# Performance work log

Measured on AMD Instinct MI355X. Metric: run time of the kernel, lower is better.

The kernel has to match this reference:

```python
import jax, jax.numpy as jnp
import numpy as np

V = 50000      # vocab_size
E = 512        # embed_size
H = 512        # hidden_size
B = 128        # batch
S = 256        # encoder seq len
MAX_OOVS = 12


def setup_inputs() -> dict:
    key = jax.random.key(0)
    ks = jax.random.split(key, 18)
    s = 0.05
    embed_table = jax.random.normal(ks[4], (V, E), jnp.float32) * s
    embed_table = embed_table.at[0].set(0.0)  # padding_idx=0
    return {
        'input_idx':   jax.random.randint(ks[0], (B,), 0, V),
        'encoded':     jax.random.normal(ks[1], (B, S, H), jnp.float32),
        'encoded_idx': jax.random.randint(ks[2], (B, S), 0, V),
        'prev_state':  jax.random.normal(ks[3], (B, H), jnp.float32),
        'weighted':    jnp.zeros((B, 1, H), jnp.float32),
        'embed_table': embed_table,
        'Ws_w':    jax.random.normal(ks[5], (H, H), jnp.float32) * s,
        'Ws_b':    jnp.zeros((H,), jnp.float32),
        'gru_Wih': jax.random.normal(ks[6], (3 * H, E + H), jnp.float32) * s,
        'gru_Whh': jax.random.normal(ks[7], (3 * H, H), jnp.float32) * s,
        'gru_bih': jnp.zeros((3 * H,), jnp.float32),
        'gru_bhh': jnp.zeros((3 * H,), jnp.float32),
        'attn_W':  jax.random.normal(ks[8], (H, 2 * H), jnp.float32) * s,
        'attn_b':  jnp.zeros((H,), jnp.float32),
        'attn_v':  jax.random.normal(ks[9], (H,), jnp.float32) * s,
        'Wo_w':    jax.random.normal(ks[10], (V, 2 * H), jnp.float32) * s,
        'Wo_b':    jnp.zeros((V,), jnp.float32),
        'Wc_w':    jax.random.normal(ks[11], (2 * H, H), jnp.float32) * s,
        'Wc_b':    jnp.zeros((2 * H,), jnp.float32),
    }


def copy_decoder_fwd(input_idx, encoded, encoded_idx, prev_state, weighted,
                     embed_table, Ws_w, Ws_b, gru_Wih, gru_Whh, gru_bih, gru_bhh,
                     attn_W, attn_b, attn_v, Wo_w, Wo_b, Wc_w, Wc_b):
    b, seq, hidden = encoded.shape
    vocab = Wo_w.shape[0]
    dt = encoded.dtype

    # order == 0 branch: project prev_state, zero the weighted context
    prev = prev_state @ Ws_w.T + Ws_b                      # (b, h)
    wtd = jnp.zeros((b, hidden), dt)                       # (b, h)

    # GRU single step (PyTorch gate layout: r, z, n)
    x = jnp.concatenate([embed_table[input_idx], wtd], axis=1)  # (b, e+h)
    gi = x @ gru_Wih.T + gru_bih                           # (b, 3h)
    gh = prev @ gru_Whh.T + gru_bhh                        # (b, 3h)
    i_r, i_z, i_n = jnp.split(gi, 3, axis=1)
    h_r, h_z, h_n = jnp.split(gh, 3, axis=1)
    r = jax.nn.sigmoid(i_r + h_r)
    z = jax.nn.sigmoid(i_z + h_z)
    n = jnp.tanh(i_n + r * h_n)
    state = (1.0 - z) * n + z * prev                       # (b, h), == rnn_output

    # 'concat' attention: softmax_seq(v . tanh(W[h; enc] + b))
    h_exp = jnp.broadcast_to(state[:, None, :], (b, seq, hidden))
    energy = jnp.tanh(jnp.concatenate([h_exp, encoded], axis=-1) @ attn_W.T + attn_b)
    attn_w = jax.nn.softmax(energy @ attn_v, axis=1)       # (b, seq)
    context = jnp.einsum('bs,bsh->bh', attn_w, encoded)    # (b, h)

    # generation scores
    score_g = jnp.concatenate([state, context], axis=1) @ Wo_w.T + Wo_b  # (b, V)

    # copy scores
    sc = jnp.tanh(encoded @ Wc_w.T + Wc_b)                 # (b, seq, 2h)
    score_c = jnp.einsum('bsk,bk->bs', sc, jnp.concatenate([state, context], axis=1))
    score_c = score_c + jnp.where(encoded_idx == 0, -1000.0, 0.0).astype(dt)

    # joint softmax over vocab + seq
    probs = jax.nn.softmax(jnp.concatenate([score_g, score_c], axis=1), axis=1)
    prob_g = probs[:, :vocab]                              # (b, V)
    prob_c = probs[:, vocab:]                              # (b, seq)
    prob_c_given = prob_c / jnp.sum(prob_c)                # global-scalar normalization (faithful)

    # pad generation probs with small oov mass
    vext = vocab + MAX_OOVS
    prob_g_ext = jnp.concatenate(
        [prob_g, jnp.full((b, MAX_OOVS), 1e-4, dt)], axis=1)  # (b, V+oov)

    # copy -> vocab scatter-add (replaces dense one-hot + bmm)
    batch_ids = jnp.broadcast_to(jnp.arange(b)[:, None], (b, seq))
    prob_c_to_g = jnp.zeros((b, vext), dt).at[batch_ids, encoded_idx].add(prob_c)

    out = (prob_g_ext + prob_c_to_g)[:, None, :]           # (b, 1, V+oov)

    # positions in source equal to the current input token
    ind = (encoded_idx == input_idx[:, None]).astype(dt)   # (b, seq)
    ssum = ind.sum(axis=1, keepdims=True)
    ind = jnp.where(ssum > 1.0, ind / ssum, ind)
    attn2 = prob_c_given * ind                             # (b, seq)
    weighted_new = jnp.einsum('bs,bsh->bh', attn2, encoded)[:, None, :]  # (b, 1, h)

    return out, state, weighted_new


def reference(input_idx, encoded, encoded_idx, prev_state, weighted,
              embed_table, Ws_w, Ws_b, gru_Wih, gru_Whh, gru_bih, gru_bhh,
              attn_W, attn_b, attn_v, Wo_w, Wo_b, Wc_w, Wc_b):
    return copy_decoder_fwd(input_idx, encoded, encoded_idx, prev_state, weighted,
                            embed_table, Ws_w, Ws_b, gru_Wih, gru_Whh, gru_bih, gru_bhh,
                            attn_W, attn_b, attn_v, Wo_w, Wo_b, Wc_w, Wc_b)
```

## Files before the change

kernel.cpp:

```cpp
#include <hip/hip_runtime.h>
#include <hip/hip_bf16.h>
#include <math.h>

#define BB 128
#define SS 256
#define HH 512
#define VV 50000
#define VEXT 50012

typedef __bf16 bf16x8 __attribute__((ext_vector_type(8)));
typedef float f32x4 __attribute__((ext_vector_type(4)));

__device__ __forceinline__ float fast_tanh(float x) {
  float e = __expf(2.0f * x);
  return 1.0f - 2.0f / (e + 1.0f);
}
__device__ __forceinline__ float fast_sigmoid(float x) {
  return 1.0f / (1.0f + __expf(-x));
}
__device__ __forceinline__ bf16x8 cvt8(const float* p) {
  float4 a = *(const float4*)p;
  float4 b = *(const float4*)(p + 4);
  bf16x8 r;
  r[0] = (__bf16)a.x; r[1] = (__bf16)a.y; r[2] = (__bf16)a.z; r[3] = (__bf16)a.w;
  r[4] = (__bf16)b.x; r[5] = (__bf16)b.y; r[6] = (__bf16)b.z; r[7] = (__bf16)b.w;
  return r;
}

__global__ void k_pack_w(const float* __restrict__ src, int ldw, int coff, int icount,
                         __hip_bfloat16* __restrict__ dst) {
  int i = blockIdx.x * 256 + threadIdx.x;
  if (i >= icount) return;
  int l = i & 63, ks = (i >> 6) & 15, tile = i >> 10;
  int m = l & 15, q = l >> 4;
  const float* p = src + (size_t)(tile * 16 + m) * ldw + coff + ks * 32 + q * 8;
  *(bf16x8*)(dst + (size_t)i * 8) = cvt8(p);
}

__global__ void k_pack_enc(const float* __restrict__ enc, __hip_bfloat16* __restrict__ epk) {
  int i = blockIdx.x * 256 + threadIdx.x;
  int l = i & 63, ks = (i >> 6) & 15, st = (i >> 10) & 15, b = i >> 14;
  int m = l & 15, q = l >> 4;
  const float* p = enc + ((size_t)b * SS + st * 16 + m) * HH + ks * 32 + q * 8;
  *(bf16x8*)(epk + (size_t)i * 8) = cvt8(p);
}

template <int LDB, bool GATHER>
__global__ __launch_bounds__(256, 2) void k_gemm_bt(
    const float* __restrict__ A, const float* __restrict__ B,
    const float* __restrict__ bias, float* __restrict__ C, int ldc,
    const int* __restrict__ gidx) {
  __shared__ __hip_bfloat16 ylds[128 * 72];
  const int t = threadIdx.x;
  const int l = t & 63, w = t >> 6;
  const int m = l & 15, q = l >> 4;
  const int n = blockIdx.x * 64 + w * 16 + m;
  const float* wrow = B + (size_t)n * LDB;
  f32x4 acc[8];
#pragma unroll
  for (int mt = 0; mt < 8; ++mt) acc[mt] = (f32x4){0.f, 0.f, 0.f, 0.f};

  for (int kt = 0; kt < 512; kt += 64) {
    __syncthreads();
#pragma unroll
    for (int i = 0; i < 8; ++i) {
      int f = t + i * 256;
      int row = f >> 4, c4 = f & 15;
      const float* arow;
      if (GATHER)
        arow = A + (size_t)gidx[row] * 512;
      else
        arow = A + (size_t)row * 512;
      float4 v = *(const float4*)(arow + kt + c4 * 4);
      __hip_bfloat16* d = ylds + row * 72 + c4 * 4;
      d[0] = __float2bfloat16(v.x); d[1] = __float2bfloat16(v.y);
      d[2] = __float2bfloat16(v.z); d[3] = __float2bfloat16(v.w);
    }
    __syncthreads();
#pragma unroll
    for (int ksl = 0; ksl < 2; ++ksl) {
      bf16x8 bfr = cvt8(wrow + kt + ksl * 32 + q * 8);
#pragma unroll
      for (int mt = 0; mt < 8; ++mt) {
        bf16x8 af = *(const bf16x8*)(ylds + (mt * 16 + m) * 72 + ksl * 32 + q * 8);
        acc[mt] = __builtin_amdgcn_mfma_f32_16x16x32_bf16(af, bfr, acc[mt], 0, 0, 0);
      }
    }
  }
  float bv = bias[n];
#pragma unroll
  for (int mt = 0; mt < 8; ++mt) {
#pragma unroll
    for (int r = 0; r < 4; ++r) {
      int rowm = mt * 16 + q * 4 + r;
      C[(size_t)rowm * ldc + n] = acc[mt][r] + bv;
    }
  }
}

__global__ void k_gates(const float* __restrict__ gi, const float* __restrict__ gh,
                        const float* __restrict__ prevv, float* __restrict__ state,
                        float* __restrict__ state_out) {
  int i = blockIdx.x * 256 + threadIdx.x;
  int b = i >> 9, h = i & 511;
  const float* gib = gi + (size_t)b * 1536;
  const float* ghb = gh + (size_t)b * 1536;
  float ir = gib[h], iz = gib[512 + h], inn = gib[1024 + h];
  float hr = ghb[h], hz = ghb[512 + h], hn = ghb[1024 + h];
  float r = fast_sigmoid(ir + hr);
  float z = fast_sigmoid(iz + hz);
  float n = fast_tanh(inn + r * hn);
  float st = (1.f - z) * n + z * prevv[i];
  state[i] = st;
  state_out[i] = st;
}

template <int NTOT, int MODE>
__global__ __launch_bounds__(256, 3) void k_fused(
    const __hip_bfloat16* __restrict__ epack, const __hip_bfloat16* __restrict__ wpk,
    const float* __restrict__ biasA, const float* __restrict__ multA,
    const int* __restrict__ enc_idx, float* __restrict__ out) {
  const int b = blockIdx.x, s0 = blockIdx.y * 32, t = threadIdx.x;
  const int l = t & 63, w = t >> 6;
  const int wm = w & 1, wn = w >> 1;
  const int m = l & 15, q = l >> 4;
  __shared__ float bias_l[NTOT];
  __shared__ float mult_l[NTOT];
  __shared__ float red[2][32];
  const float* bias_base = (MODE == 0) ? biasA + (size_t)b * HH : biasA;
  const float* mult_base = (MODE == 0) ? multA : multA + (size_t)b * 1024;
  for (int i = t; i < NTOT; i += 256) {
    bias_l[i] = bias_base[i];
    mult_l[i] = mult_base[i];
  }
  const int st = blockIdx.y * 2 + wm;
  const __hip_bfloat16* ep = epack + ((size_t)(b * 16 + st) * 16) * 512 + (size_t)l * 8;
  bf16x8 afr[16];
#pragma unroll
  for (int ks = 0; ks < 16; ++ks) afr[ks] = *(const bf16x8*)(ep + ks * 512);
  __syncthreads();

  float part[4] = {0.f, 0.f, 0.f, 0.f};
  for (int nb = 0; nb < NTOT; nb += 32) {
    const __hip_bfloat16* wp = wpk + ((size_t)((nb >> 4) + wn) * 16) * 512 + (size_t)l * 8;
    bf16x8 bfr[16];
#pragma unroll
    for (int ks = 0; ks < 16; ++ks) bfr[ks] = *(const bf16x8*)(wp + ks * 512);
    f32x4 a0 = {0.f, 0.f, 0.f, 0.f}, a1 = a0, a2 = a0, a3 = a0;
#pragma unroll
    for (int j = 0; j < 4; ++j) {
      a0 = __builtin_amdgcn_mfma_f32_16x16x32_bf16(afr[j], bfr[j], a0, 0, 0, 0);
      a1 = __builtin_amdgcn_mfma_f32_16x16x32_bf16(afr[4 + j], bfr[4 + j], a1, 0, 0, 0);
      a2 = __builtin_amdgcn_mfma_f32_16x16x32_bf16(afr[8 + j], bfr[8 + j], a2, 0, 0, 0);
      a3 = __builtin_amdgcn_mfma_f32_16x16x32_bf16(afr[12 + j], bfr[12 + j], a3, 0, 0, 0);
    }
    f32x4 acc = (a0 + a1) + (a2 + a3);
    const int n = nb + wn * 16 + m;
    float bias = bias_l[n];
    float mul = mult_l[n];
#pragma unroll
    for (int r = 0; r < 4; ++r) part[r] += fast_tanh(acc[r] + bias) * mul;
  }
#pragma unroll
  for (int r = 0; r < 4; ++r) {
    part[r] += __shfl_xor(part[r], 1, 64);
    part[r] += __shfl_xor(part[r], 2, 64);
    part[r] += __shfl_xor(part[r], 4, 64);
    part[r] += __shfl_xor(part[r], 8, 64);
  }
  if (m == 0) {
#pragma unroll
    for (int r = 0; r < 4; ++r) red[wn][wm * 16 + q * 4 + r] = part[r];
  }
  __syncthreads();
  if (t < 32) {
    float v = red[0][t] + red[1][t];
    int s = s0 + t;
    if (MODE == 1 && enc_idx[b * SS + s] == 0) v -= 1000.0f;
    out[b * SS + s] = v;
  }
}

__global__ __launch_bounds__(256, 2) void k_score_g_mfma(
    const float* __restrict__ y, const float* __restrict__ Wo_w,
    const float* __restrict__ Wo_b, float* __restrict__ sg) {
  __shared__ __hip_bfloat16 ylds[128 * 72];
  const int t = threadIdx.x;
  const int l = t & 63, w = t >> 6;
  const int m = l & 15, q = l >> 4;
  const int nb = blockIdx.x * 64;
  const int n = nb + w * 16 + m;
  const int n_ld = (n < VV) ? n : (VV - 1);
  const float* wrow = Wo_w + (size_t)n_ld * 1024;
  f32x4 acc[8];
#pragma unroll
  for (int mt = 0; mt < 8; ++mt) acc[mt] = (f32x4){0.f, 0.f, 0.f, 0.f};

  for (int kt = 0; kt < 1024; kt += 64) {
    __syncthreads();
#pragma unroll
    for (int i = 0; i < 8; ++i) {
      int f = t + i * 256;
      int row = f >> 4, c4 = f & 15;
      float4 v = *(const float4*)(y + (size_t)row * 1024 + kt + c4 * 4);
      __hip_bfloat16* d = ylds + row * 72 + c4 * 4;
      d[0] = __float2bfloat16(v.x); d[1] = __float2bfloat16(v.y);
      d[2] = __float2bfloat16(v.z); d[3] = __float2bfloat16(v.w);
    }
    __syncthreads();
#pragma unroll
    for (int ksl = 0; ksl < 2; ++ksl) {
      bf16x8 bfr = cvt8(wrow + kt + ksl * 32 + q * 8);
#pragma unroll
      for (int mt = 0; mt < 8; ++mt) {
        bf16x8 af = *(const bf16x8*)(ylds + (mt * 16 + m) * 72 + ksl * 32 + q * 8);
        acc[mt] = __builtin_amdgcn_mfma_f32_16x16x32_bf16(af, bfr, acc[mt], 0, 0, 0);
      }
    }
  }
  if (n < VV) {
    float bias = Wo_b[n];
#pragma unroll
    for (int mt = 0; mt < 8; ++mt) {
#pragma unroll
      for (int r = 0; r < 4; ++r) {
        int rowm = mt * 16 + q * 4 + r;
        sg[(size_t)rowm * VV + n] = acc[mt][r] + bias;
      }
    }
  }
}

__global__ void k_attn_softmax(const float* __restrict__ score, float* __restrict__ aw) {
  const int b = blockIdx.x, t = threadIdx.x;
  __shared__ float rbuf[8];
  __shared__ float MS[2];
  float x = score[b * SS + t];
  float m = x;
  for (int off = 32; off > 0; off >>= 1) m = fmaxf(m, __shfl_xor(m, off, 64));
  if ((t & 63) == 0) rbuf[t >> 6] = m;
  __syncthreads();
  if (t == 0) MS[0] = fmaxf(fmaxf(rbuf[0], rbuf[1]), fmaxf(rbuf[2], rbuf[3]));
  __syncthreads();
  float e = __expf(x - MS[0]);
  float s = e;
  for (int off = 32; off > 0; off >>= 1) s += __shfl_xor(s, off, 64);
  if ((t & 63) == 0) rbuf[4 + (t >> 6)] = s;
  __syncthreads();
  if (t == 0) MS[1] = rbuf[4] + rbuf[5] + rbuf[6] + rbuf[7];
  __syncthreads();
  aw[b * SS + t] = e / MS[1];
}

__global__ void k_context(const float* __restrict__ aw, const float* __restrict__ enc,
                          const float* __restrict__ state, float* __restrict__ y) {
  const int b = blockIdx.x, hc = blockIdx.y, t = threadIdx.x;
  __shared__ float aws[SS];
  aws[t] = aw[b * SS + t];
  aws[t + 128] = aw[b * SS + t + 128];
  __syncthreads();
  int h = hc * 128 + t;
  float acc = 0.f;
  for (int s = 0; s < SS; ++s) acc += aws[s] * enc[((size_t)b * SS + s) * HH + h];
  y[(size_t)b * 1024 + HH + h] = acc;
  y[(size_t)b * 1024 + h] = state[b * HH + h];
}

__global__ void k_rowstat_part(const float* __restrict__ sg,
                               float* __restrict__ pmax, float* __restrict__ psum) {
  const int b = blockIdx.x, c = blockIdx.y, t = threadIdx.x;
  __shared__ float rbuf[8];
  __shared__ float MS[1];
  const float* row = sg + (size_t)b * VV;
  const int base = c * 6250, end = base + 6250;
  float m = -1e30f;
  for (int i = base + t; i < end; i += 256) m = fmaxf(m, row[i]);
  for (int off = 32; off > 0; off >>= 1) m = fmaxf(m, __shfl_xor(m, off, 64));
  if ((t & 63) == 0) rbuf[t >> 6] = m;
  __syncthreads();
  if (t == 0) MS[0] = fmaxf(fmaxf(rbuf[0], rbuf[1]), fmaxf(rbuf[2], rbuf[3]));
  __syncthreads();
  float M = MS[0];
  float s = 0.f;
  for (int i = base + t; i < end; i += 256) s += __expf(row[i] - M);
  for (int off = 32; off > 0; off >>= 1) s += __shfl_xor(s, off, 64);
  if ((t & 63) == 0) rbuf[4 + (t >> 6)] = s;
  __syncthreads();
  if (t == 0) {
    pmax[b * 8 + c] = M;
    psum[b * 8 + c] = rbuf[4] + rbuf[5] + rbuf[6] + rbuf[7];
  }
}

__global__ void k_rowstat_final(const float* __restrict__ pmax, const float* __restrict__ psum,
                                const float* __restrict__ sc,
                                float* __restrict__ rmax, float* __restrict__ rsum) {
  const int b = blockIdx.x, t = threadIdx.x;
  float m = -1e30f;
  if (t < 8) m = pmax[b * 8 + t];
  for (int i = t; i < SS; i += 64) m = fmaxf(m, sc[b * SS + i]);
  for (int off = 32; off > 0; off >>= 1) m = fmaxf(m, __shfl_xor(m, off, 64));
  float M = m;
  float s = 0.f;
  if (t < 8) s = psum[b * 8 + t] * __expf(pmax[b * 8 + t] - M);
  for (int i = t; i < SS; i += 64) s += __expf(sc[b * SS + i] - M);
  for (int off = 32; off > 0; off >>= 1) s += __shfl_xor(s, off, 64);
  if (t == 0) {
    rmax[b] = M;
    rsum[b] = s;
  }
}

__global__ void k_write_probg(const float* __restrict__ sg,
                              const float* __restrict__ rmax,
                              const float* __restrict__ rsum,
                              float* __restrict__ out) {
  int i = blockIdx.x * 256 + threadIdx.x;
  const int total = BB * VEXT;
  if (i >= total) return;
  int b = i / VEXT;
  int v = i - b * VEXT;
  float val;
  if (v < VV)
    val = __expf(sg[(size_t)b * VV + v] - rmax[b]) / rsum[b];
  else
    val = 1e-4f;
  out[i] = val;
}

__global__ void k_probc(const float* __restrict__ sc,
                        const int* __restrict__ enc_idx,
                        const float* __restrict__ rmax,
                        const float* __restrict__ rsum,
                        float* __restrict__ prob_c,
                        float* __restrict__ out,
                        float* __restrict__ pc_total) {
  const int b = blockIdx.x, t = threadIdx.x;
  __shared__ float rbuf[8];
  float pc = __expf(sc[b * SS + t] - rmax[b]) / rsum[b];
  prob_c[b * SS + t] = pc;
  atomicAdd(&out[(size_t)b * VEXT + enc_idx[b * SS + t]], pc);
  float s = pc;
  for (int off = 32; off > 0; off >>= 1) s += __shfl_down(s, off, 64);
  if ((t & 63) == 0) rbuf[t >> 6] = s;
  __syncthreads();
  if (t == 0) atomicAdd(pc_total, rbuf[0] + rbuf[1] + rbuf[2] + rbuf[3]);
}

__global__ void k_weighted(const int* __restrict__ enc_idx,
                           const int* __restrict__ input_idx,
                           const float* __restrict__ prob_c,
                           const float* __restrict__ pc_total,
                           const float* __restrict__ enc,
                           float* __restrict__ wout) {
  const int b = blockIdx.x, hc = blockIdx.y, t = threadIdx.x;
  __shared__ float f[SS];
  __shared__ float rb[2];
  const int idx_in = input_idx[b];
  int m0 = (enc_idx[b * SS + t] == idx_in) ? 1 : 0;
  int m1 = (enc_idx[b * SS + t + 128] == idx_in) ? 1 : 0;
  float lsum = (float)(m0 + m1);
  for (int off = 32; off > 0; off >>= 1) lsum += __shfl_xor(lsum, off, 64);
  if ((t & 63) == 0) rb[t >> 6] = lsum;
  __syncthreads();
  float tot = rb[0] + rb[1];
  float norm = (tot > 1.0f) ? 1.0f / tot : 1.0f;
  float inv_pct = 1.0f / pc_total[0];
  f[t] = m0 ? prob_c[b * SS + t] * inv_pct * norm : 0.f;
  f[t + 128] = m1 ? prob_c[b * SS + t + 128] * inv_pct * norm : 0.f;
  __syncthreads();
  int h = hc * 128 + t;
  float acc = 0.f;
  for (int s = 0; s < SS; ++s) acc += f[s] * enc[((size_t)b * SS + s) * HH + h];
  wout[b * HH + h] = acc;
}

extern "C" void kernel_launch(void* const* d_in, const int* in_sizes, int n_in,
                              void* d_out, int out_size, void* d_ws, size_t ws_size,
                              hipStream_t stream) {
  const int* input_idx = (const int*)d_in[0];
  const float* encoded = (const float*)d_in[1];
  const int* encoded_idx = (const int*)d_in[2];
  const float* prev_state = (const float*)d_in[3];
  const float* embed = (const float*)d_in[5];
  const float* Ws_w = (const float*)d_in[6];
  const float* Ws_b = (const float*)d_in[7];
  const float* gWih = (const float*)d_in[8];
  const float* gWhh = (const float*)d_in[9];
  const float* gbih = (const float*)d_in[10];
  const float* gbhh = (const float*)d_in[11];
  const float* attn_W = (const float*)d_in[12];
  const float* attn_b = (const float*)d_in[13];
  const float* attn_v = (const float*)d_in[14];
  const float* Wo_w = (const float*)d_in[15];
  const float* Wo_b = (const float*)d_in[16];
  const float* Wc_w = (const float*)d_in[17];
  const float* Wc_b = (const float*)d_in[18];

  float* out = (float*)d_out;
  float* out_state = out + (size_t)BB * VEXT;
  float* out_weighted = out_state + BB * HH;

  float* ws = (float*)d_ws;
  float* prevv = ws;
  float* state = prevv + BB * HH;
  float* hW = state + BB * HH;
  float* ascore = hW + BB * HH;
  float* aw = ascore + BB * SS;
  float* y = aw + BB * SS;
  float* sg = y + BB * 1024;
  float* sc = sg + (size_t)BB * VV;
  float* prob_c = sc + BB * SS;
  float* pmax = prob_c + BB * SS;
  float* psum = pmax + BB * 8;
  float* rmax = psum + BB * 8;
  float* rsum = rmax + BB;
  float* pc_total = rsum + BB;
  __hip_bfloat16* wc_bf = (__hip_bfloat16*)(pc_total + 64);
  __hip_bfloat16* wa_bf = wc_bf + (size_t)1024 * HH;
  __hip_bfloat16* epack = wa_bf + (size_t)512 * HH;

  float* gi = sg;
  float* gh = sg + BB * 1536;

  hipMemsetAsync(pc_total, 0, sizeof(float), stream);

  k_pack_w<<<256, 256, 0, stream>>>(Wc_w, 512, 0, 1024 * 64, wc_bf);
  k_pack_w<<<128, 256, 0, stream>>>(attn_W, 1024, 512, 512 * 64, wa_bf);
  k_pack_enc<<<8192, 256, 0, stream>>>(encoded, epack);

  k_gemm_bt<512, false><<<8, 256, 0, stream>>>(prev_state, Ws_w, Ws_b, prevv, 512, nullptr);
  k_gemm_bt<1024, true><<<24, 256, 0, stream>>>(embed, gWih, gbih, gi, 1536, input_idx);
  k_gemm_bt<512, false><<<24, 256, 0, stream>>>(prevv, gWhh, gbhh, gh, 1536, nullptr);
  k_gates<<<256, 256, 0, stream>>>(gi, gh, prevv, state, out_state);
  k_gemm_bt<1024, false><<<8, 256, 0, stream>>>(state, attn_W, attn_b, hW, 512, nullptr);

  k_fused<HH, 0><<<dim3(BB, 8), 256, 0, stream>>>(epack, wa_bf, hW, attn_v,
                                                  nullptr, ascore);
  k_attn_softmax<<<BB, 256, 0, stream>>>(ascore, aw);
  k_context<<<dim3(BB, 4), 128, 0, stream>>>(aw, encoded, state, y);

  k_score_g_mfma<<<(VV + 63) / 64, 256, 0, stream>>>(y, Wo_w, Wo_b, sg);
  k_fused<1024, 1><<<dim3(BB, 8), 256, 0, stream>>>(epack, wc_bf, Wc_b, y,
                                                    encoded_idx, sc);

  k_rowstat_part<<<dim3(BB, 8), 256, 0, stream>>>(sg, pmax, psum);
  k_rowstat_final<<<BB, 64, 0, stream>>>(pmax, psum, sc, rmax, rsum);
  k_write_probg<<<(BB * VEXT + 255) / 256, 256, 0, stream>>>(sg, rmax, rsum, out);
  k_probc<<<BB, 256, 0, stream>>>(sc, encoded_idx, rmax, rsum, prob_c, out, pc_total);
  k_weighted<<<dim3(BB, 4), 128, 0, stream>>>(encoded_idx, input_idx, prob_c, pc_total,
                                              encoded, out_weighted);
}
```

Baseline: 731.8 us.

## Fuse vocab-softmax partial stats into score GEMM epilogue and pre-pack y

The vocab score GEMM now computes per-block row max and sum-of-exp in its epilogue, writing 782 partials per row. A single merge kernel combines them with the copy scores, which removes the separate pass that re-read the full 128x50000 score matrix. The y operand is pre-packed into MFMA fragment layout in bf16, so the GEMM reads it directly instead of staging it through LDS with barriers. The three pack kernels and the memset are merged into one launch. The costs are a larger epilogue with extra barriers and shuffles, and a larger partial-stat workspace.

```diff
diff --git a/kernel.cpp b/kernel.cpp
--- a/kernel.cpp
+++ b/kernel.cpp
@@ -7,6 +7,8 @@
 #define HH 512
 #define VV 50000
 #define VEXT 50012
+#define NBLK 782
+#define PST 784
 
 typedef __bf16 bf16x8 __attribute__((ext_vector_type(8)));
 typedef float f32x4 __attribute__((ext_vector_type(4)));
@@ -27,22 +29,40 @@
   return r;
 }
 
-__global__ void k_pack_w(const float* __restrict__ src, int ldw, int coff, int icount,
-                         __hip_bfloat16* __restrict__ dst) {
+__global__ void k_pack_all(const float* __restrict__ Wc_w, const float* __restrict__ attn_W,
+                           const float* __restrict__ enc,
+                           __hip_bfloat16* __restrict__ wc_bf,
+                           __hip_bfloat16* __restrict__ wa_bf,
+                           __hip_bfloat16* __restrict__ epk,
+                           float* __restrict__ pc_total) {
   int i = blockIdx.x * 256 + threadIdx.x;
-  if (i >= icount) return;
-  int l = i & 63, ks = (i >> 6) & 15, tile = i >> 10;
+  if (blockIdx.x == 0 && threadIdx.x == 0) pc_total[0] = 0.f;
+  if (i < 65536) {
+    int l = i & 63, ks = (i >> 6) & 15, tile = i >> 10;
+    int m = l & 15, q = l >> 4;
+    const float* p = Wc_w + (size_t)(tile * 16 + m) * 512 + ks * 32 + q * 8;
+    *(bf16x8*)(wc_bf + (size_t)i * 8) = cvt8(p);
+  } else if (i < 98304) {
+    int j = i - 65536;
+    int l = j & 63, ks = (j >> 6) & 15, tile = j >> 10;
+    int m = l & 15, q = l >> 4;
+    const float* p = attn_W + (size_t)(tile * 16 + m) * 1024 + 512 + ks * 32 + q * 8;
+    *(bf16x8*)(wa_bf + (size_t)j * 8) = cvt8(p);
+  } else if (i < 98304 + 2097152) {
+    int j = i - 98304;
+    int l = j & 63, ks = (j >> 6) & 15, st = (j >> 10) & 15, b = j >> 14;
+    int m = l & 15, q = l >> 4;
+    const float* p = enc + ((size_t)b * SS + st * 16 + m) * HH + ks * 32 + q * 8;
+    *(bf16x8*)(epk + (size_t)j * 8) = cvt8(p);
+  }
+}
+
+__global__ void k_pack_y(const float* __restrict__ y, __hip_bfloat16* __restrict__ ypk) {
+  int i = blockIdx.x * 256 + threadIdx.x;
+  int l = i & 63, ks = (i >> 6) & 31, tile = i >> 11;
   int m = l & 15, q = l >> 4;
-  const float* p = src + (size_t)(tile * 16 + m) * ldw + coff + ks * 32 + q * 8;
-  *(bf16x8*)(dst + (size_t)i * 8) = cvt8(p);
-}
-
-__global__ void k_pack_enc(const float* __restrict__ enc, __hip_bfloat16* __restrict__ epk) {
-  int i = blockIdx.x * 256 + threadIdx.x;
-  int l = i & 63, ks = (i >> 6) & 15, st = (i >> 10) & 15, b = i >> 14;
-  int m = l & 15, q = l >> 4;
-  const float* p = enc + ((size_t)b * SS + st * 16 + m) * HH + ks * 32 + q * 8;
-  *(bf16x8*)(epk + (size_t)i * 8) = cvt8(p);
+  const float* p = y + (size_t)(tile * 16 + m) * 1024 + ks * 32 + q * 8;
+  *(bf16x8*)(ypk + (size_t)i * 8) = cvt8(p);
 }
 
 template <int LDB, bool GATHER>
@@ -181,53 +201,104 @@
   }
 }
 
-__global__ __launch_bounds__(256, 2) void k_score_g_mfma(
-    const float* __restrict__ y, const float* __restrict__ Wo_w,
-    const float* __restrict__ Wo_b, float* __restrict__ sg) {
-  __shared__ __hip_bfloat16 ylds[128 * 72];
+__global__ __launch_bounds__(256, 4) void k_score_g2(
+    const __hip_bfloat16* __restrict__ ypk, const float* __restrict__ Wo_w,
+    const float* __restrict__ Wo_b, float* __restrict__ sg,
+    float* __restrict__ ppmax, float* __restrict__ ppsum) {
   const int t = threadIdx.x;
   const int l = t & 63, w = t >> 6;
   const int m = l & 15, q = l >> 4;
-  const int nb = blockIdx.x * 64;
-  const int n = nb + w * 16 + m;
+  const int blk = blockIdx.x;
+  const int n = blk * 64 + w * 16 + m;
   const int n_ld = (n < VV) ? n : (VV - 1);
   const float* wrow = Wo_w + (size_t)n_ld * 1024;
   f32x4 acc[8];
 #pragma unroll
   for (int mt = 0; mt < 8; ++mt) acc[mt] = (f32x4){0.f, 0.f, 0.f, 0.f};
 
-  for (int kt = 0; kt < 1024; kt += 64) {
-    __syncthreads();
-#pragma unroll
-    for (int i = 0; i < 8; ++i) {
-      int f = t + i * 256;
-      int row = f >> 4, c4 = f & 15;
-      float4 v = *(const float4*)(y + (size_t)row * 1024 + kt + c4 * 4);
-      __hip_bfloat16* d = ylds + row * 72 + c4 * 4;
-      d[0] = __float2bfloat16(v.x); d[1] = __float2bfloat16(v.y);
-      d[2] = __float2bfloat16(v.z); d[3] = __float2bfloat16(v.w);
-    }
-    __syncthreads();
-#pragma unroll
-    for (int ksl = 0; ksl < 2; ++ksl) {
-      bf16x8 bfr = cvt8(wrow + kt + ksl * 32 + q * 8);
-#pragma unroll
-      for (int mt = 0; mt < 8; ++mt) {
-        bf16x8 af = *(const bf16x8*)(ylds + (mt * 16 + m) * 72 + ksl * 32 + q * 8);
-        acc[mt] = __builtin_amdgcn_mfma_f32_16x16x32_bf16(af, bfr, acc[mt], 0, 0, 0);
-      }
-    }
-  }
-  if (n < VV) {
-    float bias = Wo_b[n];
+  for (int ks = 0; ks < 32; ++ks) {
+    bf16x8 bfr = cvt8(wrow + ks * 32 + q * 8);
 #pragma unroll
     for (int mt = 0; mt < 8; ++mt) {
-#pragma unroll
-      for (int r = 0; r < 4; ++r) {
-        int rowm = mt * 16 + q * 4 + r;
-        sg[(size_t)rowm * VV + n] = acc[mt][r] + bias;
-      }
-    }
+      bf16x8 af = *(const bf16x8*)(ypk + (((size_t)mt * 32 + ks) * 64 + l) * 8);
+      acc[mt] = __builtin_amdgcn_mfma_f32_16x16x32_bf16(af, bfr, acc[mt], 0, 0, 0);
+    }
+  }
+
+  float bv = (n < VV) ? Wo_b[n] : 0.f;
+#pragma unroll
+  for (int mt = 0; mt < 8; ++mt) {
+#pragma unroll
+    for (int r = 0; r < 4; ++r) {
+      float v = acc[mt][r] + bv;
+      if (n < VV)
+        sg[(size_t)(mt * 16 + q * 4 + r) * VV + n] = v;
+      else
+        v = -1e30f;
+      acc[mt][r] = v;
+    }
+  }
+
+  __shared__ float redA[4][128];
+  __shared__ float MS[128];
+#pragma unroll
+  for (int mt = 0; mt < 8; ++mt) {
+#pragma unroll
+    for (int r = 0; r < 4; ++r) {
+      float mx = acc[mt][r];
+      mx = fmaxf(mx, __shfl_xor(mx, 1, 64));
+      mx = fmaxf(mx, __shfl_xor(mx, 2, 64));
+      mx = fmaxf(mx, __shfl_xor(mx, 4, 64));
+      mx = fmaxf(mx, __shfl_xor(mx, 8, 64));
+      if (m == 0) redA[w][mt * 16 + q * 4 + r] = mx;
+    }
+  }
+  __syncthreads();
+  if (t < 128)
+    MS[t] = fmaxf(fmaxf(redA[0][t], redA[1][t]), fmaxf(redA[2][t], redA[3][t]));
+  __syncthreads();
+#pragma unroll
+  for (int mt = 0; mt < 8; ++mt) {
+#pragma unroll
+    for (int r = 0; r < 4; ++r) {
+      float s = __expf(acc[mt][r] - MS[mt * 16 + q * 4 + r]);
+      s += __shfl_xor(s, 1, 64);
+      s += __shfl_xor(s, 2, 64);
+      s += __shfl_xor(s, 4, 64);
+      s += __shfl_xor(s, 8, 64);
+      if (m == 0) redA[w][mt * 16 + q * 4 + r] = s;
+    }
+  }
+  __syncthreads();
+  if (t < 128) {
+    ppmax[(size_t)t * PST + blk] = MS[t];
+    ppsum[(size_t)t * PST + blk] = redA[0][t] + redA[1][t] + redA[2][t] + redA[3][t];
+  }
+}
+
+__global__ void k_rowstat_merge(const float* __restrict__ ppmax, const float* __restrict__ ppsum,
+                                const float* __restrict__ sc,
+                                float* __restrict__ rmax, float* __restrict__ rsum) {
+  const int row = blockIdx.x, t = threadIdx.x;
+  __shared__ float rb[8];
+  __shared__ float MS[1];
+  float mrow = sc[row * SS + t];
+  for (int i = t; i < NBLK; i += 256) mrow = fmaxf(mrow, ppmax[(size_t)row * PST + i]);
+  for (int off = 32; off > 0; off >>= 1) mrow = fmaxf(mrow, __shfl_xor(mrow, off, 64));
+  if ((t & 63) == 0) rb[t >> 6] = mrow;
+  __syncthreads();
+  if (t == 0) MS[0] = fmaxf(fmaxf(rb[0], rb[1]), fmaxf(rb[2], rb[3]));
+  __syncthreads();
+  float M = MS[0];
+  float s = __expf(sc[row * SS + t] - M);
+  for (int i = t; i < NBLK; i += 256)
+    s += ppsum[(size_t)row * PST + i] * __expf(ppmax[(size_t)row * PST + i] - M);
+  for (int off = 32; off > 0; off >>= 1) s += __shfl_xor(s, off, 64);
+  if ((t & 63) == 0) rb[4 + (t >> 6)] = s;
+  __syncthreads();
+  if (t == 0) {
+    rmax[row] = M;
+    rsum[row] = rb[4] + rb[5] + rb[6] + rb[7];
   }
 }
 
@@ -264,51 +335,6 @@
   for (int s = 0; s < SS; ++s) acc += aws[s] * enc[((size_t)b * SS + s) * HH + h];
   y[(size_t)b * 1024 + HH + h] = acc;
   y[(size_t)b * 1024 + h] = state[b * HH + h];
-}
-
-__global__ void k_rowstat_part(const float* __restrict__ sg,
-                               float* __restrict__ pmax, float* __restrict__ psum) {
-  const int b = blockIdx.x, c = blockIdx.y, t = threadIdx.x;
-  __shared__ float rbuf[8];
-  __shared__ float MS[1];
-  const float* row = sg + (size_t)b * VV;
-  const int base = c * 6250, end = base + 6250;
-  float m = -1e30f;
-  for (int i = base + t; i < end; i += 256) m = fmaxf(m, row[i]);
-  for (int off = 32; off > 0; off >>= 1) m = fmaxf(m, __shfl_xor(m, off, 64));
-  if ((t & 63) == 0) rbuf[t >> 6] = m;
-  __syncthreads();
-  if (t == 0) MS[0] = fmaxf(fmaxf(rbuf[0], rbuf[1]), fmaxf(rbuf[2], rbuf[3]));
-  __syncthreads();
-  float M = MS[0];
-  float s = 0.f;
-  for (int i = base + t; i < end; i += 256) s += __expf(row[i] - M);
-  for (int off = 32; off > 0; off >>= 1) s += __shfl_xor(s, off, 64);
-  if ((t & 63) == 0) rbuf[4 + (t >> 6)] = s;
-  __syncthreads();
-  if (t == 0) {
-    pmax[b * 8 + c] = M;
-    psum[b * 8 + c] = rbuf[4] + rbuf[5] + rbuf[6] + rbuf[7];
-  }
-}
-
-__global__ void k_rowstat_final(const float* __restrict__ pmax, const float* __restrict__ psum,
-                                const float* __restrict__ sc,
-                                float* __restrict__ rmax, float* __restrict__ rsum) {
-  const int b = blockIdx.x, t = threadIdx.x;
-  float m = -1e30f;
-  if (t < 8) m = pmax[b * 8 + t];
-  for (int i = t; i < SS; i += 64) m = fmaxf(m, sc[b * SS + i]);
-  for (int off = 32; off > 0; off >>= 1) m = fmaxf(m, __shfl_xor(m, off, 64));
-  float M = m;
-  float s = 0.f;
-  if (t < 8) s = psum[b * 8 + t] * __expf(pmax[b * 8 + t] - M);
-  for (int i = t; i < SS; i += 64) s += __expf(sc[b * SS + i] - M);
-  for (int off = 32; off > 0; off >>= 1) s += __shfl_xor(s, off, 64);
-  if (t == 0) {
-    rmax[b] = M;
-    rsum[b] = s;
-  }
 }
 
 __global__ void k_write_probg(const float* __restrict__ sg,
@@ -411,23 +437,20 @@
   float* sg = y + BB * 1024;
   float* sc = sg + (size_t)BB * VV;
   float* prob_c = sc + BB * SS;
-  float* pmax = prob_c + BB * SS;
-  float* psum = pmax + BB * 8;
-  float* rmax = psum + BB * 8;
+  float* rmax = prob_c + BB * SS;
   float* rsum = rmax + BB;
   float* pc_total = rsum + BB;
-  __hip_bfloat16* wc_bf = (__hip_bfloat16*)(pc_total + 64);
+  float* ppmax = pc_total + 64;
+  float* ppsum = ppmax + (size_t)BB * PST;
+  __hip_bfloat16* wc_bf = (__hip_bfloat16*)(ppsum + (size_t)BB * PST);
   __hip_bfloat16* wa_bf = wc_bf + (size_t)1024 * HH;
   __hip_bfloat16* epack = wa_bf + (size_t)512 * HH;
+  __hip_bfloat16* ypk = epack + (size_t)BB * SS * HH;
 
   float* gi = sg;
   float* gh = sg + BB * 1536;
 
-  hipMemsetAsync(pc_total, 0, sizeof(float), stream);
-
-  k_pack_w<<<256, 256, 0, stream>>>(Wc_w, 512, 0, 1024 * 64, wc_bf);
-  k_pack_w<<<128, 256, 0, stream>>>(attn_W, 1024, 512, 512 * 64, wa_bf);
-  k_pack_enc<<<8192, 256, 0, stream>>>(encoded, epack);
+  k_pack_all<<<8576, 256, 0, stream>>>(Wc_w, attn_W, encoded, wc_bf, wa_bf, epack, pc_total);
 
   k_gemm_bt<512, false><<<8, 256, 0, stream>>>(prev_state, Ws_w, Ws_b, prevv, 512, nullptr);
   k_gemm_bt<1024, true><<<24, 256, 0, stream>>>(embed, gWih, gbih, gi, 1536, input_idx);
@@ -439,13 +462,13 @@
                                                   nullptr, ascore);
   k_attn_softmax<<<BB, 256, 0, stream>>>(ascore, aw);
   k_context<<<dim3(BB, 4), 128, 0, stream>>>(aw, encoded, state, y);
-
-  k_score_g_mfma<<<(VV + 63) / 64, 256, 0, stream>>>(y, Wo_w, Wo_b, sg);
+  k_pack_y<<<64, 256, 0, stream>>>(y, ypk);
+
+  k_score_g2<<<NBLK, 256, 0, stream>>>(ypk, Wo_w, Wo_b, sg, ppmax, ppsum);
   k_fused<1024, 1><<<dim3(BB, 8), 256, 0, stream>>>(epack, wc_bf, Wc_b, y,
                                                     encoded_idx, sc);
 
-  k_rowstat_part<<<dim3(BB, 8), 256, 0, stream>>>(sg, pmax, psum);
-  k_rowstat_final<<<BB, 64, 0, stream>>>(pmax, psum, sc, rmax, rsum);
+  k_rowstat_merge<<<BB, 256, 0, stream>>>(ppmax, ppsum, sc, rmax, rsum);
   k_write_probg<<<(BB * VEXT + 255) / 256, 256, 0, stream>>>(sg, rmax, rsum, out);
   k_probc<<<BB, 256, 0, stream>>>(sc, encoded_idx, rmax, rsum, prob_c, out, pc_total);
   k_weighted<<<dim3(BB, 4), 128, 0, stream>>>(encoded_idx, input_idx, prob_c, pc_total,
```

Result: no change. 718.0 us (-1.9%).
